# Kernel tuning notes

Measured on AMD Instinct MI355X. Metric: run time of the kernel, lower is better.

Reference implementation:

```python
import jax, jax.numpy as jnp
import numpy as np

D_MODEL = 1024
H = 16
D_K = D_MODEL // H


def setup_inputs() -> dict:
    key = jax.random.key(0)
    ks = jax.random.split(key, 12)
    B, S = 4, 2048
    q = jax.random.normal(ks[0], (B, S, D_MODEL), jnp.float32)
    k = jax.random.normal(ks[1], (B, S, D_MODEL), jnp.float32)
    v = jax.random.normal(ks[2], (B, S, D_MODEL), jnp.float32)
    # causal mask, broadcastable to [B, H, S, S]; mask==0 positions are blocked
    mask = jnp.tril(jnp.ones((S, S), jnp.int32))[None, None]
    scale = 1.0 / np.sqrt(D_MODEL)
    Wq = jax.random.normal(ks[3], (D_MODEL, D_MODEL), jnp.float32) * scale
    bq = jax.random.normal(ks[4], (D_MODEL,), jnp.float32) * 0.02
    Wk = jax.random.normal(ks[5], (D_MODEL, D_MODEL), jnp.float32) * scale
    bk = jax.random.normal(ks[6], (D_MODEL,), jnp.float32) * 0.02
    Wv = jax.random.normal(ks[7], (D_MODEL, D_MODEL), jnp.float32) * scale
    bv = jax.random.normal(ks[8], (D_MODEL,), jnp.float32) * 0.02
    Wo = jax.random.normal(ks[9], (D_MODEL, D_MODEL), jnp.float32) * scale
    bo = jax.random.normal(ks[10], (D_MODEL,), jnp.float32) * 0.02
    return {"q": q, "k": k, "v": v, "mask": mask,
            "Wq": Wq, "bq": bq, "Wk": Wk, "bk": bk,
            "Wv": Wv, "bv": bv, "Wo": Wo, "bo": bo}


def reference(q, k, v, mask, Wq, bq, Wk, bk, Wv, bv, Wo, bo):
    B, S, _ = q.shape
    # linear projections (torch nn.Linear: x @ W.T + b)
    query = q @ Wq.T + bq
    key = k @ Wk.T + bk
    value = v @ Wv.T + bv
    # [B, S, D] -> [B, H, S, d_k]
    def split_heads(x):
        return x.reshape(B, S, H, D_K).transpose(0, 2, 1, 3)
    query, key, value = split_heads(query), split_heads(key), split_heads(value)
    # scaled dot-product attention, scores: [B, H, S, S]
    scores = jnp.einsum('bhqd,bhkd->bhqk', query, key) / np.sqrt(D_K)
    scores = jnp.where(mask == 0, jnp.float32(-1e9), scores)
    attn = jax.nn.softmax(scores, axis=-1)
    x = jnp.einsum('bhqk,bhkd->bhqd', attn, value)  # [B, H, S, d_k]
    x = x.transpose(0, 2, 1, 3).reshape(B, S, D_MODEL)
    return x @ Wo.T + bo
```

## Files before the change

kernel.cpp:

```cpp
#include <hip/hip_runtime.h>

#define DM 1024
#define SEQ 2048
#define NH 16
#define DK 64

typedef __bf16 bf16x8 __attribute__((ext_vector_type(8)));
typedef float f32x4 __attribute__((ext_vector_type(4)));

#define QSCALE 0.1803368801111244f

__device__ inline unsigned short f2bf(float f) {
    unsigned u = __float_as_uint(f);
    u += 0x7fffu + ((u >> 16) & 1u);
    return (unsigned short)(u >> 16);
}

__device__ inline unsigned pkbf(float lo, float hi) {
    union { __bf16 h[2]; unsigned u; } r;
    r.h[0] = (__bf16)lo; r.h[1] = (__bf16)hi;
    return r.u;
}

__global__ __launch_bounds__(256) void cvt_w(const float* __restrict__ s0,
                                             const float* __restrict__ s1,
                                             const float* __restrict__ s2,
                                             const float* __restrict__ s3,
                                             unsigned short* __restrict__ d0,
                                             unsigned short* __restrict__ d1,
                                             unsigned short* __restrict__ d2,
                                             unsigned short* __restrict__ d3) {
    const float* s;
    unsigned short* d;
    switch (blockIdx.y) {
        case 0: s = s0; d = d0; break;
        case 1: s = s1; d = d1; break;
        case 2: s = s2; d = d2; break;
        default: s = s3; d = d3; break;
    }
    int i = (blockIdx.x * 256 + threadIdx.x) * 4;
    float4 v = *(const float4*)(s + i);
    ushort4 o;
    o.x = f2bf(v.x); o.y = f2bf(v.y); o.z = f2bf(v.z); o.w = f2bf(v.w);
    *(ushort4*)(d + i) = o;
}

__global__ __launch_bounds__(512) void gemm_proj(const float* __restrict__ A,
                                                 const unsigned short* __restrict__ W,
                                                 const float* __restrict__ bias,
                                                 unsigned short* __restrict__ C,
                                                 float oscale, int out_mode) {
    __shared__ unsigned short lds_a[128 * 64];
    __shared__ unsigned short lds_w[2][128 * 64];

    const int K = DM, N = DM;
    const int t = threadIdx.x;
    const int lane = t & 63;
    const int w = t >> 6;
    const int wr = w >> 1;
    const int wc = w & 1;
    const int bid = blockIdx.x;
    const int xcd = bid & 7;
    const int idx = bid >> 3;
    const int rowBase = (xcd * 8 + (idx >> 3)) * 128;
    const int colBase = (idx & 7) * 128;
    const int l15 = lane & 15;
    const int lg = lane >> 4;
    const int ar = t >> 2, aq = t & 3;
    const int NIT = K >> 6;

    f32x4 acc[2][4] = {};

    auto STAGE_W = [&](int kt, int buf) {
#pragma unroll
        for (int i = 0; i < 2; ++i) {
            const int row = (w * 2 + i) * 8 + (lane >> 3);
            const int sl = lane & 7;
            const unsigned short* src =
                W + (size_t)(colBase + row) * K + kt * 64 + ((sl ^ (row & 7)) * 8);
            __builtin_amdgcn_global_load_lds(src, &lds_w[buf][(w * 2 + i) * 512], 16, 0, 0);
        }
    };
    auto LOADA = [&](int kt, float4* rf) {
        const float* Af = A + (size_t)(rowBase + ar) * K + kt * 64 + aq * 16;
#pragma unroll
        for (int i = 0; i < 4; ++i) rf[i] = *(const float4*)(Af + i * 4);
    };
    auto WRITEA = [&](const float4* rf) {
#pragma unroll
        for (int i = 0; i < 2; ++i) {
            union { __bf16 h[8]; uint4 u; } pk;
            pk.h[0] = (__bf16)rf[2 * i].x; pk.h[1] = (__bf16)rf[2 * i].y;
            pk.h[2] = (__bf16)rf[2 * i].z; pk.h[3] = (__bf16)rf[2 * i].w;
            pk.h[4] = (__bf16)rf[2 * i + 1].x; pk.h[5] = (__bf16)rf[2 * i + 1].y;
            pk.h[6] = (__bf16)rf[2 * i + 1].z; pk.h[7] = (__bf16)rf[2 * i + 1].w;
            *(uint4*)&lds_a[ar * 64 + (((aq * 2 + i) ^ (ar & 7)) * 8)] = pk.u;
        }
    };
    auto COMPUTE = [&](int wbuf) {
#pragma unroll
        for (int kh = 0; kh < 2; ++kh) {
            bf16x8 af[2], wf[4];
#pragma unroll
            for (int m = 0; m < 2; ++m)
                af[m] = *(const bf16x8*)&lds_a[(wr * 32 + m * 16 + l15) * 64 +
                                               (((kh * 4 + lg) ^ (l15 & 7)) * 8)];
#pragma unroll
            for (int n = 0; n < 4; ++n)
                wf[n] = *(const bf16x8*)&lds_w[wbuf][(wc * 64 + n * 16 + l15) * 64 +
                                                    (((kh * 4 + lg) ^ (l15 & 7)) * 8)];
#pragma unroll
            for (int m = 0; m < 2; ++m)
#pragma unroll
                for (int n = 0; n < 4; ++n)
                    acc[m][n] = __builtin_amdgcn_mfma_f32_16x16x32_bf16(af[m], wf[n],
                                                                        acc[m][n], 0, 0, 0);
        }
    };

    float4 ra[4], rb[4];
    STAGE_W(0, 0);
    LOADA(0, ra);
    for (int kt = 0; kt < NIT; kt += 2) {
        if (kt + 1 < NIT) {
            STAGE_W(kt + 1, 1);
            LOADA(kt + 1, rb);
            asm volatile("s_waitcnt vmcnt(6)" ::: "memory");
        } else {
            asm volatile("s_waitcnt vmcnt(0)" ::: "memory");
        }
        WRITEA(ra);
        asm volatile("s_waitcnt lgkmcnt(0)" ::: "memory");
        __builtin_amdgcn_s_barrier();
        COMPUTE(0);
        __builtin_amdgcn_s_barrier();
        if (kt + 2 < NIT) {
            STAGE_W(kt + 2, 0);
            LOADA(kt + 2, ra);
            asm volatile("s_waitcnt vmcnt(6)" ::: "memory");
        } else {
            asm volatile("s_waitcnt vmcnt(0)" ::: "memory");
        }
        WRITEA(rb);
        asm volatile("s_waitcnt lgkmcnt(0)" ::: "memory");
        __builtin_amdgcn_s_barrier();
        COMPUTE(1);
        __builtin_amdgcn_s_barrier();
    }

#pragma unroll
    for (int m = 0; m < 2; ++m) {
        int row = rowBase + wr * 32 + m * 16 + lg * 4;
#pragma unroll
        for (int n = 0; n < 4; ++n) {
            int col = colBase + wc * 64 + n * 16 + l15;
            float bv = bias[col];
            if (out_mode == 2) {
                const int bh = (row >> 11) * NH + (col >> 6);
                const int dloc = col & 63;
                const int s = row & (SEQ - 1);
                ushort4 o;
                o.x = f2bf(acc[m][n][0] + bv);
                o.y = f2bf(acc[m][n][1] + bv);
                o.z = f2bf(acc[m][n][2] + bv);
                o.w = f2bf(acc[m][n][3] + bv);
                *(ushort4*)(C + ((size_t)bh * DK + dloc) * SEQ + s) = o;
            } else {
#pragma unroll
                for (int j = 0; j < 4; ++j)
                    C[(size_t)(row + j) * N + col] = f2bf((acc[m][n][j] + bv) * oscale);
            }
        }
    }
}

__global__ __launch_bounds__(512) void gemm_out(const unsigned short* __restrict__ A,
                                                const unsigned short* __restrict__ W,
                                                const float* __restrict__ bias,
                                                float* __restrict__ C) {
    __shared__ unsigned short lds_a[2][128 * 64];
    __shared__ unsigned short lds_w[2][128 * 64];

    const int K = DM, N = DM;
    const int t = threadIdx.x;
    const int lane = t & 63;
    const int w = t >> 6;
    const int wr = w >> 1;
    const int wc = w & 1;
    const int bid = blockIdx.x;
    const int xcd = bid & 7;
    const int idx = bid >> 3;
    const int rowBase = (xcd * 8 + (idx >> 3)) * 128;
    const int colBase = (idx & 7) * 128;
    const int l15 = lane & 15;
    const int lg = lane >> 4;
    const int NIT = K >> 6;

    f32x4 acc[2][4] = {};

    auto STAGE = [&](const unsigned short* M0, unsigned short* ldsb, int kt) {
#pragma unroll
        for (int i = 0; i < 2; ++i) {
            const int row = (w * 2 + i) * 8 + (lane >> 3);
            const int sl = lane & 7;
            const unsigned short* src =
                M0 + (size_t)row * K + kt * 64 + ((sl ^ (row & 7)) * 8);
            __builtin_amdgcn_global_load_lds(src, ldsb + (w * 2 + i) * 512, 16, 0, 0);
        }
    };
    auto COMPUTE = [&](int buf) {
#pragma unroll
        for (int kh = 0; kh < 2; ++kh) {
            bf16x8 af[2], wf[4];
#pragma unroll
            for (int m = 0; m < 2; ++m)
                af[m] = *(const bf16x8*)&lds_a[buf][(wr * 32 + m * 16 + l15) * 64 +
                                                   (((kh * 4 + lg) ^ (l15 & 7)) * 8)];
#pragma unroll
            for (int n = 0; n < 4; ++n)
                wf[n] = *(const bf16x8*)&lds_w[buf][(wc * 64 + n * 16 + l15) * 64 +
                                                   (((kh * 4 + lg) ^ (l15 & 7)) * 8)];
#pragma unroll
            for (int m = 0; m < 2; ++m)
#pragma unroll
                for (int n = 0; n < 4; ++n)
                    acc[m][n] = __builtin_amdgcn_mfma_f32_16x16x32_bf16(af[m], wf[n],
                                                                        acc[m][n], 0, 0, 0);
        }
    };

    const unsigned short* Arow = A + (size_t)rowBase * K;
    const unsigned short* Wrow = W + (size_t)colBase * K;
    STAGE(Wrow, lds_w[0], 0);
    STAGE(Arow, lds_a[0], 0);
    for (int kt = 0; kt < NIT; ++kt) {
        const int cur = kt & 1;
        if (kt + 1 < NIT) {
            STAGE(Wrow, lds_w[cur ^ 1], kt + 1);
            STAGE(Arow, lds_a[cur ^ 1], kt + 1);
            asm volatile("s_waitcnt vmcnt(4)" ::: "memory");
        } else {
            asm volatile("s_waitcnt vmcnt(0)" ::: "memory");
        }
        __builtin_amdgcn_s_barrier();
        COMPUTE(cur);
        __builtin_amdgcn_s_barrier();
    }

#pragma unroll
    for (int m = 0; m < 2; ++m) {
        int row = rowBase + wr * 32 + m * 16 + lg * 4;
#pragma unroll
        for (int n = 0; n < 4; ++n) {
            int col = colBase + wc * 64 + n * 16 + l15;
            float bv = bias[col];
#pragma unroll
            for (int j = 0; j < 4; ++j)
                C[(size_t)(row + j) * N + col] = acc[m][n][j] + bv;
        }
    }
}

__global__ __launch_bounds__(256) void attn(const unsigned short* __restrict__ Q,
                                            const unsigned short* __restrict__ K,
                                            const unsigned short* __restrict__ Vt,
                                            unsigned short* __restrict__ X) {
    __shared__ unsigned short k_lds[2][128 * 64];
    __shared__ unsigned short v_lds[2][64 * 128];

    const int t = threadIdx.x;
    const int lane = t & 63;
    const int w = t >> 6;
    const int l15 = lane & 15, lg = lane >> 4;
    const int c4 = (lane >> 4) & 1, c5 = (lane >> 5) & 1;

    const int orig = blockIdx.x;
    const int flat = (orig & 7) * 128 + (orig >> 3);
    const int bh = flat >> 4;
    const int pr = flat & 15;
    const int b = bh >> 4, h = bh & 15;

    const unsigned short* Qb = Q + (size_t)b * SEQ * DM + h * DK;
    const unsigned short* Kb = K + (size_t)b * SEQ * DM + h * DK;
    const unsigned short* Vb = Vt + (size_t)bh * DK * SEQ;

    const int ksr = t >> 3;
    const int ksc8 = (t & 7) * 8;
    const int kxo = (ksr & 7) * 8;
    const int vsr = t >> 2;
    const int vq = t & 3;
    const int vxo = vsr & 15;
    const int xork = (l15 & 7) * 8;

    union { unsigned short us[8]; bf16x8 v; } ou;
#pragma unroll
    for (int i = 0; i < 8; ++i) ou.us[i] = 0x3F80;
    const bf16x8 onesf = ou.v;

    bf16x8 kr[4], vr[4];
    int gp = 0;

    auto LOADT = [&](int kv0) {
#pragma unroll
        for (int i = 0; i < 4; ++i)
            kr[i] = *(const bf16x8*)(Kb + (size_t)(kv0 + i * 32 + ksr) * DM + ksc8);
#pragma unroll
        for (int j = 0; j < 4; ++j)
            vr[j] = *(const bf16x8*)(Vb + (size_t)vsr * SEQ + kv0 + (j * 4 + vq) * 8);
    };

    LOADT(0);

    for (int task = 0; task < 2; ++task) {
        const int qt = task ? 31 - pr : pr;
        const int qrow0 = qt * 64 + w * 16;
        const int qg = qrow0 + l15;

        const bf16x8 qf0 = *(const bf16x8*)(Qb + (size_t)(qrow0 + l15) * DM + lg * 8);
        const bf16x8 qf1 = *(const bf16x8*)(Qb + (size_t)(qrow0 + l15) * DM + lg * 8 + 32);

        f32x4 acc[4] = {};
        f32x4 accS = {};
        const int nt = (qt + 2) >> 1;

        for (int tile = 0; tile < nt; ++tile) {
            const int kv0 = tile << 7;
            unsigned short* kl = k_lds[gp & 1];
            unsigned short* vl = v_lds[gp & 1];
#pragma unroll
            for (int i = 0; i < 4; ++i)
                *(bf16x8*)&kl[(i * 32 + ksr) * 64 + (ksc8 ^ kxo)] = kr[i];
#pragma unroll
            for (int j = 0; j < 4; ++j)
                *(bf16x8*)&vl[vsr * 128 + (((j * 4 + vq) ^ vxo) * 8)] = vr[j];
            __syncthreads();

            if (tile + 1 < nt)
                LOADT((tile + 1) << 7);
            else if (task == 0)
                LOADT(0);

#pragma unroll
            for (int hh = 0; hh < 2; ++hh) {
                const int kvb = kv0 + hh * 64;
                if (kvb > qrow0 + 15) break;

                f32x4 st[4];
#pragma unroll
                for (int s = 0; s < 4; ++s) {
                    const int rb2 = (hh * 64 + s * 16 + l15) * 64;
                    bf16x8 ka = *(const bf16x8*)&kl[rb2 + ((lg * 8) ^ xork)];
                    bf16x8 kb2 = *(const bf16x8*)&kl[rb2 + ((32 + lg * 8) ^ xork)];
                    f32x4 z = {};
                    z = __builtin_amdgcn_mfma_f32_16x16x32_bf16(ka, qf0, z, 0, 0, 0);
                    st[s] = __builtin_amdgcn_mfma_f32_16x16x32_bf16(kb2, qf1, z, 0, 0, 0);
                }

                bf16x8 vf[4][2];
#pragma unroll
                for (int d = 0; d < 4; ++d) {
                    const int base = (d * 16 + l15) * 128;
                    vf[d][0] = *(const bf16x8*)&vl[base + (((hh * 8 + lg) ^ l15) * 8)];
                    vf[d][1] = *(const bf16x8*)&vl[base + (((hh * 8 + 4 + lg) ^ l15) * 8)];
                }

                float ps[16];
                if (kvb + 63 > qrow0) {
#pragma unroll
                    for (int s = 0; s < 4; ++s)
#pragma unroll
                        for (int j = 0; j < 4; ++j) {
                            const bool ok = kvb + s * 16 + 4 * lg + j <= qg;
                            ps[s * 4 + j] = ok ? exp2f(st[s][j]) : 0.0f;
                        }
                } else {
#pragma unroll
                    for (int s = 0; s < 4; ++s)
#pragma unroll
                        for (int j = 0; j < 4; ++j)
                            ps[s * 4 + j] = exp2f(st[s][j]);
                }

                bf16x8 pf[2];
#pragma unroll
                for (int hq = 0; hq < 2; ++hq) {
                    const float* p8 = &ps[hq * 8];
                    unsigned wsp[2][2];
#pragma unroll
                    for (int s = 0; s < 2; ++s)
#pragma unroll
                        for (int p2 = 0; p2 < 2; ++p2)
                            wsp[s][p2] = pkbf(p8[s * 4 + 2 * p2], p8[s * 4 + 2 * p2 + 1]);
                    unsigned n0[2], n1[2];
#pragma unroll
                    for (int p2 = 0; p2 < 2; ++p2) {
                        unsigned snd = c5 ? wsp[0][p2] : wsp[1][p2];
                        unsigned exch = __shfl_xor((int)snd, 32, 64);
                        n0[p2] = c5 ? exch : wsp[0][p2];
                        n1[p2] = c5 ? wsp[1][p2] : exch;
                    }
                    unsigned f0[2], f1[2];
#pragma unroll
                    for (int p2 = 0; p2 < 2; ++p2) {
                        unsigned snd = c4 ? n0[p2] : n1[p2];
                        unsigned exch = __shfl_xor((int)snd, 16, 64);
                        f0[p2] = c4 ? exch : n0[p2];
                        f1[p2] = c4 ? n1[p2] : exch;
                    }
                    union { unsigned u[4]; bf16x8 v; } pu;
                    pu.u[0] = f0[0]; pu.u[1] = f0[1]; pu.u[2] = f1[0]; pu.u[3] = f1[1];
                    pf[hq] = pu.v;
                }

#pragma unroll
                for (int d = 0; d < 4; ++d) {
                    acc[d] = __builtin_amdgcn_mfma_f32_16x16x32_bf16(vf[d][0], pf[0], acc[d], 0, 0, 0);
                    acc[d] = __builtin_amdgcn_mfma_f32_16x16x32_bf16(vf[d][1], pf[1], acc[d], 0, 0, 0);
                }
                accS = __builtin_amdgcn_mfma_f32_16x16x32_bf16(onesf, pf[0], accS, 0, 0, 0);
                accS = __builtin_amdgcn_mfma_f32_16x16x32_bf16(onesf, pf[1], accS, 0, 0, 0);
            }
            gp++;
        }

        const float inv = 1.0f / accS[0];
#pragma unroll
        for (int d = 0; d < 4; ++d) {
            ushort4 o;
            o.x = f2bf(acc[d][0] * inv);
            o.y = f2bf(acc[d][1] * inv);
            o.z = f2bf(acc[d][2] * inv);
            o.w = f2bf(acc[d][3] * inv);
            *(ushort4*)&X[(size_t)(b * SEQ + qg) * DM + h * DK + d * 16 + 4 * lg] = o;
        }
    }
}

extern "C" void kernel_launch(void* const* d_in, const int* in_sizes, int n_in,
                              void* d_out, int out_size, void* d_ws, size_t ws_size,
                              hipStream_t stream) {
    const float* q  = (const float*)d_in[0];
    const float* k  = (const float*)d_in[1];
    const float* v  = (const float*)d_in[2];
    const float* Wq = (const float*)d_in[4];
    const float* bq = (const float*)d_in[5];
    const float* Wk = (const float*)d_in[6];
    const float* bk = (const float*)d_in[7];
    const float* Wv = (const float*)d_in[8];
    const float* bv = (const float*)d_in[9];
    const float* Wo = (const float*)d_in[10];
    const float* bo = (const float*)d_in[11];

    const size_t NEL = (size_t)4 * SEQ * DM;
    const size_t WEL = (size_t)DM * DM;
    unsigned short* Qp  = (unsigned short*)d_ws;
    unsigned short* Kp  = Qp + NEL;
    unsigned short* Vp  = Kp + NEL;
    unsigned short* Vt  = Vp + NEL;
    unsigned short* Wob = Vt + NEL;
    unsigned short* Xp  = Vp;
    unsigned short* Wqb = (unsigned short*)d_out;
    unsigned short* Wkb = Wqb + WEL;
    unsigned short* Wvb = Wkb + WEL;

    hipLaunchKernelGGL(cvt_w, dim3(1024, 4), dim3(256), 0, stream, Wq, Wk, Wv, Wo,
                       Wqb, Wkb, Wvb, Wob);
    hipLaunchKernelGGL(gemm_proj, dim3(512), dim3(512), 0, stream, q, Wqb, bq, Qp,
                       QSCALE, 0);
    hipLaunchKernelGGL(gemm_proj, dim3(512), dim3(512), 0, stream, k, Wkb, bk, Kp,
                       1.0f, 0);
    hipLaunchKernelGGL(gemm_proj, dim3(512), dim3(512), 0, stream, v, Wvb, bv, Vt,
                       1.0f, 2);
    hipLaunchKernelGGL(attn, dim3(1024), dim3(256), 0, stream, Qp, Kp, Vt, Xp);
    hipLaunchKernelGGL(gemm_out, dim3(512), dim3(512), 0, stream, Xp, Wob, bo,
                       (float*)d_out);
}
```

Baseline: 223.2 us.

## Shrink attention KV tile from 128 to 64 rows and clamp exponent

Cuts the attention kernel's per-iteration K/V tile from 128 to 64 keys. That halves the LDS buffers and register staging and simplifies the V layout to the same swizzle as K. Each tile now runs one unconditional 64-key block, with no inner two-half loop and early break. This lowers LDS use and register pressure and should improve occupancy, at the cost of twice as many barriers and tile iterations. It also clamps the exp2 argument to 30 to guard against overflow in the unnormalized softmax.

```diff
diff --git a/kernel.cpp b/kernel.cpp
--- a/kernel.cpp
+++ b/kernel.cpp
@@ -265,8 +265,8 @@
                                             const unsigned short* __restrict__ K,
                                             const unsigned short* __restrict__ Vt,
                                             unsigned short* __restrict__ X) {
-    __shared__ unsigned short k_lds[2][128 * 64];
-    __shared__ unsigned short v_lds[2][64 * 128];
+    __shared__ unsigned short k_lds[2][64 * 64];
+    __shared__ unsigned short v_lds[2][64 * 64];
 
     const int t = threadIdx.x;
     const int lane = t & 63;
@@ -284,12 +284,9 @@
     const unsigned short* Kb = K + (size_t)b * SEQ * DM + h * DK;
     const unsigned short* Vb = Vt + (size_t)bh * DK * SEQ;
 
-    const int ksr = t >> 3;
-    const int ksc8 = (t & 7) * 8;
-    const int kxo = (ksr & 7) * 8;
-    const int vsr = t >> 2;
-    const int vq = t & 3;
-    const int vxo = vsr & 15;
+    const int sr = t >> 3;
+    const int sc8 = (t & 7) * 8;
+    const int sxo = (sr & 7) * 8;
     const int xork = (l15 & 7) * 8;
 
     union { unsigned short us[8]; bf16x8 v; } ou;
@@ -297,16 +294,14 @@
     for (int i = 0; i < 8; ++i) ou.us[i] = 0x3F80;
     const bf16x8 onesf = ou.v;
 
-    bf16x8 kr[4], vr[4];
+    bf16x8 kr0, kr1, vr0, vr1;
     int gp = 0;
 
     auto LOADT = [&](int kv0) {
-#pragma unroll
-        for (int i = 0; i < 4; ++i)
-            kr[i] = *(const bf16x8*)(Kb + (size_t)(kv0 + i * 32 + ksr) * DM + ksc8);
-#pragma unroll
-        for (int j = 0; j < 4; ++j)
-            vr[j] = *(const bf16x8*)(Vb + (size_t)vsr * SEQ + kv0 + (j * 4 + vq) * 8);
+        kr0 = *(const bf16x8*)(Kb + (size_t)(kv0 + sr) * DM + sc8);
+        kr1 = *(const bf16x8*)(Kb + (size_t)(kv0 + 32 + sr) * DM + sc8);
+        vr0 = *(const bf16x8*)(Vb + (size_t)sr * SEQ + kv0 + sc8);
+        vr1 = *(const bf16x8*)(Vb + (size_t)(32 + sr) * SEQ + kv0 + sc8);
     };
 
     LOADT(0);
@@ -321,105 +316,97 @@
 
         f32x4 acc[4] = {};
         f32x4 accS = {};
-        const int nt = (qt + 2) >> 1;
+        const int nt = qt + 1;
 
         for (int tile = 0; tile < nt; ++tile) {
-            const int kv0 = tile << 7;
+            const int kv0 = tile << 6;
             unsigned short* kl = k_lds[gp & 1];
             unsigned short* vl = v_lds[gp & 1];
-#pragma unroll
-            for (int i = 0; i < 4; ++i)
-                *(bf16x8*)&kl[(i * 32 + ksr) * 64 + (ksc8 ^ kxo)] = kr[i];
-#pragma unroll
-            for (int j = 0; j < 4; ++j)
-                *(bf16x8*)&vl[vsr * 128 + (((j * 4 + vq) ^ vxo) * 8)] = vr[j];
+            *(bf16x8*)&kl[sr * 64 + (sc8 ^ sxo)] = kr0;
+            *(bf16x8*)&kl[(sr + 32) * 64 + (sc8 ^ sxo)] = kr1;
+            *(bf16x8*)&vl[sr * 64 + (sc8 ^ sxo)] = vr0;
+            *(bf16x8*)&vl[(sr + 32) * 64 + (sc8 ^ sxo)] = vr1;
             __syncthreads();
 
             if (tile + 1 < nt)
-                LOADT((tile + 1) << 7);
+                LOADT((tile + 1) << 6);
             else if (task == 0)
                 LOADT(0);
 
+            f32x4 st[4];
+#pragma unroll
+            for (int s = 0; s < 4; ++s) {
+                const int rb2 = (s * 16 + l15) * 64;
+                bf16x8 ka = *(const bf16x8*)&kl[rb2 + ((lg * 8) ^ xork)];
+                bf16x8 kb2 = *(const bf16x8*)&kl[rb2 + ((32 + lg * 8) ^ xork)];
+                f32x4 z = {};
+                z = __builtin_amdgcn_mfma_f32_16x16x32_bf16(ka, qf0, z, 0, 0, 0);
+                st[s] = __builtin_amdgcn_mfma_f32_16x16x32_bf16(kb2, qf1, z, 0, 0, 0);
+            }
+
+            bf16x8 vf[4][2];
+#pragma unroll
+            for (int d = 0; d < 4; ++d) {
+                const int rb2 = (d * 16 + l15) * 64;
+                vf[d][0] = *(const bf16x8*)&vl[rb2 + ((lg * 8) ^ xork)];
+                vf[d][1] = *(const bf16x8*)&vl[rb2 + ((32 + lg * 8) ^ xork)];
+            }
+
+            float ps[16];
+            if (kv0 + 63 > qrow0) {
+#pragma unroll
+                for (int s = 0; s < 4; ++s)
+#pragma unroll
+                    for (int j = 0; j < 4; ++j) {
+                        const bool ok = kv0 + s * 16 + 4 * lg + j <= qg;
+                        ps[s * 4 + j] = ok ? exp2f(fminf(st[s][j], 30.0f)) : 0.0f;
+                    }
+            } else {
+#pragma unroll
+                for (int s = 0; s < 4; ++s)
+#pragma unroll
+                    for (int j = 0; j < 4; ++j)
+                        ps[s * 4 + j] = exp2f(fminf(st[s][j], 30.0f));
+            }
+
+            bf16x8 pf[2];
 #pragma unroll
             for (int hh = 0; hh < 2; ++hh) {
-                const int kvb = kv0 + hh * 64;
-                if (kvb > qrow0 + 15) break;
-
-                f32x4 st[4];
-#pragma unroll
-                for (int s = 0; s < 4; ++s) {
-                    const int rb2 = (hh * 64 + s * 16 + l15) * 64;
-                    bf16x8 ka = *(const bf16x8*)&kl[rb2 + ((lg * 8) ^ xork)];
-                    bf16x8 kb2 = *(const bf16x8*)&kl[rb2 + ((32 + lg * 8) ^ xork)];
-                    f32x4 z = {};
-                    z = __builtin_amdgcn_mfma_f32_16x16x32_bf16(ka, qf0, z, 0, 0, 0);
-                    st[s] = __builtin_amdgcn_mfma_f32_16x16x32_bf16(kb2, qf1, z, 0, 0, 0);
+                const float* p8 = &ps[hh * 8];
+                unsigned wsp[2][2];
+#pragma unroll
+                for (int s = 0; s < 2; ++s)
+#pragma unroll
+                    for (int p2 = 0; p2 < 2; ++p2)
+                        wsp[s][p2] = pkbf(p8[s * 4 + 2 * p2], p8[s * 4 + 2 * p2 + 1]);
+                unsigned n0[2], n1[2];
+#pragma unroll
+                for (int p2 = 0; p2 < 2; ++p2) {
+                    unsigned snd = c5 ? wsp[0][p2] : wsp[1][p2];
+                    unsigned exch = __shfl_xor((int)snd, 32, 64);
+                    n0[p2] = c5 ? exch : wsp[0][p2];
+                    n1[p2] = c5 ? wsp[1][p2] : exch;
                 }
-
-                bf16x8 vf[4][2];
-#pragma unroll
-                for (int d = 0; d < 4; ++d) {
-                    const int base = (d * 16 + l15) * 128;
-                    vf[d][0] = *(const bf16x8*)&vl[base + (((hh * 8 + lg) ^ l15) * 8)];
-                    vf[d][1] = *(const bf16x8*)&vl[base + (((hh * 8 + 4 + lg) ^ l15) * 8)];
+                unsigned f0[2], f1[2];
+#pragma unroll
+                for (int p2 = 0; p2 < 2; ++p2) {
+                    unsigned snd = c4 ? n0[p2] : n1[p2];
+                    unsigned exch = __shfl_xor((int)snd, 16, 64);
+                    f0[p2] = c4 ? exch : n0[p2];
+                    f1[p2] = c4 ? n1[p2] : exch;
                 }
-
-                float ps[16];
-                if (kvb + 63 > qrow0) {
-#pragma unroll
-                    for (int s = 0; s < 4; ++s)
-#pragma unroll
-                        for (int j = 0; j < 4; ++j) {
-                            const bool ok = kvb + s * 16 + 4 * lg + j <= qg;
-                            ps[s * 4 + j] = ok ? exp2f(st[s][j]) : 0.0f;
-                        }
-                } else {
-#pragma unroll
-                    for (int s = 0; s < 4; ++s)
-#pragma unroll
-                        for (int j = 0; j < 4; ++j)
-                            ps[s * 4 + j] = exp2f(st[s][j]);
-                }
-
-                bf16x8 pf[2];
-#pragma unroll
-                for (int hq = 0; hq < 2; ++hq) {
-                    const float* p8 = &ps[hq * 8];
-                    unsigned wsp[2][2];
-#pragma unroll
-                    for (int s = 0; s < 2; ++s)
-#pragma unroll
-                        for (int p2 = 0; p2 < 2; ++p2)
-                            wsp[s][p2] = pkbf(p8[s * 4 + 2 * p2], p8[s * 4 + 2 * p2 + 1]);
-                    unsigned n0[2], n1[2];
-#pragma unroll
-                    for (int p2 = 0; p2 < 2; ++p2) {
-                        unsigned snd = c5 ? wsp[0][p2] : wsp[1][p2];
-                        unsigned exch = __shfl_xor((int)snd, 32, 64);
-                        n0[p2] = c5 ? exch : wsp[0][p2];
-                        n1[p2] = c5 ? wsp[1][p2] : exch;
-                    }
-                    unsigned f0[2], f1[2];
-#pragma unroll
-                    for (int p2 = 0; p2 < 2; ++p2) {
-                        unsigned snd = c4 ? n0[p2] : n1[p2];
-                        unsigned exch = __shfl_xor((int)snd, 16, 64);
-                        f0[p2] = c4 ? exch : n0[p2];
-                        f1[p2] = c4 ? n1[p2] : exch;
-                    }
-                    union { unsigned u[4]; bf16x8 v; } pu;
-                    pu.u[0] = f0[0]; pu.u[1] = f0[1]; pu.u[2] = f1[0]; pu.u[3] = f1[1];
-                    pf[hq] = pu.v;
-                }
-
-#pragma unroll
-                for (int d = 0; d < 4; ++d) {
-                    acc[d] = __builtin_amdgcn_mfma_f32_16x16x32_bf16(vf[d][0], pf[0], acc[d], 0, 0, 0);
-                    acc[d] = __builtin_amdgcn_mfma_f32_16x16x32_bf16(vf[d][1], pf[1], acc[d], 0, 0, 0);
-                }
-                accS = __builtin_amdgcn_mfma_f32_16x16x32_bf16(onesf, pf[0], accS, 0, 0, 0);
-                accS = __builtin_amdgcn_mfma_f32_16x16x32_bf16(onesf, pf[1], accS, 0, 0, 0);
-            }
+                union { unsigned u[4]; bf16x8 v; } pu;
+                pu.u[0] = f0[0]; pu.u[1] = f0[1]; pu.u[2] = f1[0]; pu.u[3] = f1[1];
+                pf[hh] = pu.v;
+            }
+
+#pragma unroll
+            for (int d = 0; d < 4; ++d) {
+                acc[d] = __builtin_amdgcn_mfma_f32_16x16x32_bf16(vf[d][0], pf[0], acc[d], 0, 0, 0);
+                acc[d] = __builtin_amdgcn_mfma_f32_16x16x32_bf16(vf[d][1], pf[1], acc[d], 0, 0, 0);
+            }
+            accS = __builtin_amdgcn_mfma_f32_16x16x32_bf16(onesf, pf[0], accS, 0, 0, 0);
+            accS = __builtin_amdgcn_mfma_f32_16x16x32_bf16(onesf, pf[1], accS, 0, 0, 0);
             gp++;
         }
 
```

After: 217.6 us. -2.5%, faster.
